# Performance work log

Hardware: AMD Instinct MI355X
Metric: run time of the kernel (lower is better)

The kernel has to match this reference:

```python
import jax, jax.numpy as jnp
import numpy as np
from jax import lax

EMBED_DIM = 512
HIDDEN_DIM = 256
OUT_DIM = HIDDEN_DIM // 2
BATCH = 32
SEQ = 4096
THRESHOLD = 1.0
DECAY = 0.95
REFRACTORY = 2.0


def setup_inputs() -> dict:
    key = jax.random.key(0)
    k1, k2, k3 = jax.random.split(key, 3)
    x = jax.random.normal(k1, (BATCH, SEQ, EMBED_DIM), dtype=jnp.float32)
    input_weights = jax.random.normal(k2, (EMBED_DIM, HIDDEN_DIM), dtype=jnp.float32) * 0.1
    hidden_weights = jax.random.normal(k3, (HIDDEN_DIM, OUT_DIM), dtype=jnp.float32) * 0.1
    return {"x": x, "input_weights": input_weights, "hidden_weights": hidden_weights}


def reference(x, input_weights, hidden_weights):
    B, S, D = x.shape
    H = input_weights.shape[1]
    dt = x.dtype
    # batch-mean then project all timesteps at once: [S, H]
    currents = jnp.einsum('sd,dh->sh', x.mean(0), input_weights)

    def step(carry, ic):
        mem, refr = carry
        active = (refr <= 0).astype(dt)
        mem = DECAY * mem + ic * active
        spikes = (mem >= THRESHOLD).astype(dt)
        mem = mem * (1.0 - spikes)
        refr = jnp.maximum(refr - 1.0, 0.0) + spikes * REFRACTORY
        return (mem, refr), spikes

    init = (jnp.zeros((H,), dt), jnp.zeros((H,), dt))
    _, spikes = lax.scan(step, init, currents)  # spikes: [S, H]
    out = spikes @ hidden_weights               # [S, OUT]
    out_mean = out.mean(0)                      # mean over timesteps
    # original repeats the (batch-independent) output across the batch
    return jnp.broadcast_to(out_mean, (B, out_mean.shape[0]))
```

## Files before the change

kernel.cpp:

```cpp
#include <hip/hip_runtime.h>
#include <stdint.h>


#define S_LEN 4096
#define D_DIM 512
#define H_DIM 256
#define O_DIM 128
#define B_SZ  32
#define TS    8
#define CH    64
#define NCH   (S_LEN / CH)
#define ROWS  (CH / 4)

typedef const __attribute__((address_space(1))) void  glob_void;
typedef       __attribute__((address_space(3))) void  lds_void;

__global__ __launch_bounds__(256)
void fused_mean_proj(const float4* __restrict__ x4,
                     const float*  __restrict__ iw,
                     float4*       __restrict__ cur4,
                     float*        __restrict__ out) {
    __shared__ float4 xm4[TS * D_DIM / 4];
    const int t   = threadIdx.x;
    const int s0  = blockIdx.x * TS;
    const int SD4 = S_LEN * D_DIM / 4;
    const size_t base = (size_t)s0 * (D_DIM / 4);

    if (blockIdx.x == 0) {
        for (int i = t; i < B_SZ * O_DIM; i += 256) out[i] = 0.f;
    }

    float4 acc[4];
    #pragma unroll
    for (int k = 0; k < 4; ++k) acc[k] = make_float4(0.f, 0.f, 0.f, 0.f);

    for (int b = 0; b < B_SZ; b += 2) {
        const float4* p0 = x4 + (size_t)b * SD4 + base;
        const float4* p1 = p0 + SD4;
        float4 v0[4], v1[4];
        #pragma unroll
        for (int k = 0; k < 4; ++k) v0[k] = p0[t + k * 256];
        #pragma unroll
        for (int k = 0; k < 4; ++k) v1[k] = p1[t + k * 256];
        #pragma unroll
        for (int k = 0; k < 4; ++k) {
            acc[k].x += v0[k].x; acc[k].y += v0[k].y; acc[k].z += v0[k].z; acc[k].w += v0[k].w;
            acc[k].x += v1[k].x; acc[k].y += v1[k].y; acc[k].z += v1[k].z; acc[k].w += v1[k].w;
        }
    }
    const float inv = 1.0f / (float)B_SZ;
    #pragma unroll
    for (int k = 0; k < 4; ++k) {
        float4 a = acc[k];
        a.x *= inv; a.y *= inv; a.z *= inv; a.w *= inv;
        xm4[t + k * 256] = a;
    }
    __syncthreads();

    const int h = t;
    float acc2[TS];
    #pragma unroll
    for (int ss = 0; ss < TS; ++ss) acc2[ss] = 0.f;

    for (int d4 = 0; d4 < D_DIM / 4; ++d4) {
        const int d = d4 * 4;
        float w0 = iw[(d + 0) * H_DIM + h];
        float w1 = iw[(d + 1) * H_DIM + h];
        float w2 = iw[(d + 2) * H_DIM + h];
        float w3 = iw[(d + 3) * H_DIM + h];
        #pragma unroll
        for (int ss = 0; ss < TS; ++ss) {
            float4 xv = xm4[ss * (D_DIM / 4) + d4];
            acc2[ss] += xv.x * w0 + xv.y * w1 + xv.z * w2 + xv.w * w3;
        }
    }
    const int g0 = (blockIdx.x * 2) * H_DIM + h;
    cur4[g0]         = make_float4(acc2[0], acc2[1], acc2[2], acc2[3]);
    cur4[g0 + H_DIM] = make_float4(acc2[4], acc2[5], acc2[6], acc2[7]);
}

#define LIF_STEP(IC) {                          \
    float ict = sp2 ? 0.f : (IC);               \
    float tt  = fmaf(0.95f, u, ict);            \
    u   = sp1 ? 0.f : tt;                       \
    bool sp = (u >= 1.0f);                      \
    cnt += sp ? 1 : 0;                          \
    sp2 = sp1; sp1 = sp; }

__global__ __launch_bounds__(64)
void snn_scan_out(const float4* __restrict__ cur4,
                  const float*  __restrict__ hw,
                  float*        __restrict__ out) {
    __shared__ __attribute__((aligned(16))) float4 lbuf[2][ROWS * 64];
    __shared__ float cl[64];
    const int lane  = threadIdx.x;
    const int hbase = blockIdx.x * 64;

    #pragma unroll
    for (int r = 0; r < ROWS; ++r) {
        const float4* g = cur4 + (size_t)r * H_DIM + hbase + lane;
        __builtin_amdgcn_global_load_lds((glob_void*)g,
                                         (lds_void*)&lbuf[0][r * 64 + lane], 16, 0, 0);
    }

    float u = 0.f;
    int   cnt = 0;
    bool  sp1 = false, sp2 = false;

    for (int c = 0; c < NCH; ++c) {
        __syncthreads();
        if (c + 1 < NCH) {
            #pragma unroll
            for (int r = 0; r < ROWS; ++r) {
                const float4* g = cur4 + (size_t)((c + 1) * ROWS + r) * H_DIM + hbase + lane;
                __builtin_amdgcn_global_load_lds((glob_void*)g,
                                                 (lds_void*)&lbuf[(c + 1) & 1][r * 64 + lane],
                                                 16, 0, 0);
            }
        }
        const float4* lb = lbuf[c & 1];
        float4 v[ROWS];
        #pragma unroll
        for (int r = 0; r < ROWS; ++r) v[r] = lb[r * 64 + lane];
        __builtin_amdgcn_sched_barrier(0);

        #pragma unroll
        for (int r = 0; r < ROWS; ++r) {
            LIF_STEP(v[r].x); LIF_STEP(v[r].y); LIF_STEP(v[r].z); LIF_STEP(v[r].w);
        }
    }

    __syncthreads();
    cl[lane] = (float)cnt;
    __syncthreads();
    float a0 = 0.f, a1 = 0.f;
    #pragma unroll 8
    for (int k = 0; k < 64; ++k) {
        float c = cl[k];
        const float* w = hw + (size_t)(hbase + k) * O_DIM;
        a0 = fmaf(c, w[lane], a0);
        a1 = fmaf(c, w[lane + 64], a1);
    }
    a0 *= (1.0f / (float)S_LEN);
    a1 *= (1.0f / (float)S_LEN);
    for (int b = 0; b < B_SZ; ++b) {
        atomicAdd(out + b * O_DIM + lane,      a0);
        atomicAdd(out + b * O_DIM + lane + 64, a1);
    }
}

extern "C" void kernel_launch(void* const* d_in, const int* in_sizes, int n_in,
                              void* d_out, int out_size, void* d_ws, size_t ws_size,
                              hipStream_t stream) {
    const float4* x4 = (const float4*)d_in[0];
    const float*  iw = (const float*) d_in[1];
    const float*  hw = (const float*) d_in[2];
    float* out   = (float*)d_out;
    float4* cur4 = (float4*)d_ws;

    hipLaunchKernelGGL(fused_mean_proj, dim3(S_LEN / TS), dim3(256), 0, stream,
                       x4, iw, cur4, out);
    hipLaunchKernelGGL(snn_scan_out, dim3(4), dim3(64), 0, stream,
                       cur4, hw, out);
}
```

Measured before the change: 471.5 us.

## Split batch-mean from projection and triple-buffer scan chunk loads

The fused mean+projection kernel is split in two. A wide batch_mean kernel (2048 blocks, 8 loads in flight per thread) streams x and writes the [S,D] mean to workspace. A separate proj kernel then reads it from global memory. The scan kernel moves from double to triple buffering with explicit vmcnt waits, prefetching two chunks ahead and dropping the per-chunk __syncthreads. This adds an extra launch and an 8MB intermediate round trip in exchange for more memory parallelism on the dominant 256MB read and more latency hiding in the serial scan.

```diff
diff --git a/kernel.cpp b/kernel.cpp
--- a/kernel.cpp
+++ b/kernel.cpp
@@ -7,7 +7,6 @@
 #define H_DIM 256
 #define O_DIM 128
 #define B_SZ  32
-#define TS    8
 #define CH    64
 #define NCH   (S_LEN / CH)
 #define ROWS  (CH / 4)
@@ -16,62 +15,50 @@
 typedef       __attribute__((address_space(3))) void  lds_void;
 
 __global__ __launch_bounds__(256)
-void fused_mean_proj(const float4* __restrict__ x4,
-                     const float*  __restrict__ iw,
-                     float4*       __restrict__ cur4,
-                     float*        __restrict__ out) {
-    __shared__ float4 xm4[TS * D_DIM / 4];
-    const int t   = threadIdx.x;
-    const int s0  = blockIdx.x * TS;
+void batch_mean(const float4* __restrict__ x4,
+                float4*       __restrict__ xm4,
+                float*        __restrict__ out) {
+    const int i = blockIdx.x * 256 + threadIdx.x;
+    if (blockIdx.x == 0) {
+        for (int k = threadIdx.x; k < B_SZ * O_DIM; k += 256) out[k] = 0.f;
+    }
     const int SD4 = S_LEN * D_DIM / 4;
-    const size_t base = (size_t)s0 * (D_DIM / 4);
-
-    if (blockIdx.x == 0) {
-        for (int i = t; i < B_SZ * O_DIM; i += 256) out[i] = 0.f;
-    }
-
-    float4 acc[4];
-    #pragma unroll
-    for (int k = 0; k < 4; ++k) acc[k] = make_float4(0.f, 0.f, 0.f, 0.f);
-
-    for (int b = 0; b < B_SZ; b += 2) {
-        const float4* p0 = x4 + (size_t)b * SD4 + base;
-        const float4* p1 = p0 + SD4;
-        float4 v0[4], v1[4];
+    const float4* p = x4 + i;
+    float4 acc = make_float4(0.f, 0.f, 0.f, 0.f);
+    for (int b = 0; b < B_SZ; b += 8) {
+        float4 q[8];
         #pragma unroll
-        for (int k = 0; k < 4; ++k) v0[k] = p0[t + k * 256];
+        for (int j = 0; j < 8; ++j) q[j] = p[(size_t)(b + j) * SD4];
         #pragma unroll
-        for (int k = 0; k < 4; ++k) v1[k] = p1[t + k * 256];
-        #pragma unroll
-        for (int k = 0; k < 4; ++k) {
-            acc[k].x += v0[k].x; acc[k].y += v0[k].y; acc[k].z += v0[k].z; acc[k].w += v0[k].w;
-            acc[k].x += v1[k].x; acc[k].y += v1[k].y; acc[k].z += v1[k].z; acc[k].w += v1[k].w;
+        for (int j = 0; j < 8; ++j) {
+            acc.x += q[j].x; acc.y += q[j].y; acc.z += q[j].z; acc.w += q[j].w;
         }
     }
     const float inv = 1.0f / (float)B_SZ;
+    acc.x *= inv; acc.y *= inv; acc.z *= inv; acc.w *= inv;
+    xm4[i] = acc;
+}
+
+__global__ __launch_bounds__(256)
+void proj(const float* __restrict__ xmean,
+          const float* __restrict__ iw,
+          float4*      __restrict__ cur4) {
+    const int h  = threadIdx.x;
+    const int s0 = blockIdx.x * 8;
+    float acc2[8];
     #pragma unroll
-    for (int k = 0; k < 4; ++k) {
-        float4 a = acc[k];
-        a.x *= inv; a.y *= inv; a.z *= inv; a.w *= inv;
-        xm4[t + k * 256] = a;
-    }
-    __syncthreads();
+    for (int ss = 0; ss < 8; ++ss) acc2[ss] = 0.f;
 
-    const int h = t;
-    float acc2[TS];
-    #pragma unroll
-    for (int ss = 0; ss < TS; ++ss) acc2[ss] = 0.f;
-
-    for (int d4 = 0; d4 < D_DIM / 4; ++d4) {
-        const int d = d4 * 4;
+    const float* xr = xmean + (size_t)s0 * D_DIM;
+    for (int d = 0; d < D_DIM; d += 4) {
         float w0 = iw[(d + 0) * H_DIM + h];
         float w1 = iw[(d + 1) * H_DIM + h];
         float w2 = iw[(d + 2) * H_DIM + h];
         float w3 = iw[(d + 3) * H_DIM + h];
         #pragma unroll
-        for (int ss = 0; ss < TS; ++ss) {
-            float4 xv = xm4[ss * (D_DIM / 4) + d4];
-            acc2[ss] += xv.x * w0 + xv.y * w1 + xv.z * w2 + xv.w * w3;
+        for (int ss = 0; ss < 8; ++ss) {
+            const float* xp = xr + ss * D_DIM + d;
+            acc2[ss] += xp[0] * w0 + xp[1] * w1 + xp[2] * w2 + xp[3] * w3;
         }
     }
     const int g0 = (blockIdx.x * 2) * H_DIM + h;
@@ -87,38 +74,45 @@
     cnt += sp ? 1 : 0;                          \
     sp2 = sp1; sp1 = sp; }
 
+__device__ __forceinline__ void stage_chunk(const float4* __restrict__ cur4,
+                                            float4* dst, int c, int hbase, int lane) {
+    #pragma unroll
+    for (int r = 0; r < ROWS; ++r) {
+        const float4* g = cur4 + (size_t)(c * ROWS + r) * H_DIM + hbase + lane;
+        __builtin_amdgcn_global_load_lds((glob_void*)g,
+                                         (lds_void*)&dst[r * 64 + lane], 16, 0, 0);
+    }
+}
+
 __global__ __launch_bounds__(64)
 void snn_scan_out(const float4* __restrict__ cur4,
                   const float*  __restrict__ hw,
                   float*        __restrict__ out) {
-    __shared__ __attribute__((aligned(16))) float4 lbuf[2][ROWS * 64];
+    __shared__ __attribute__((aligned(16))) float4 lbuf[3][ROWS * 64];
     __shared__ float cl[64];
     const int lane  = threadIdx.x;
     const int hbase = blockIdx.x * 64;
 
-    #pragma unroll
-    for (int r = 0; r < ROWS; ++r) {
-        const float4* g = cur4 + (size_t)r * H_DIM + hbase + lane;
-        __builtin_amdgcn_global_load_lds((glob_void*)g,
-                                         (lds_void*)&lbuf[0][r * 64 + lane], 16, 0, 0);
-    }
+    stage_chunk(cur4, lbuf[0], 0, hbase, lane);
+    stage_chunk(cur4, lbuf[1], 1, hbase, lane);
 
     float u = 0.f;
     int   cnt = 0;
     bool  sp1 = false, sp2 = false;
 
     for (int c = 0; c < NCH; ++c) {
-        __syncthreads();
-        if (c + 1 < NCH) {
-            #pragma unroll
-            for (int r = 0; r < ROWS; ++r) {
-                const float4* g = cur4 + (size_t)((c + 1) * ROWS + r) * H_DIM + hbase + lane;
-                __builtin_amdgcn_global_load_lds((glob_void*)g,
-                                                 (lds_void*)&lbuf[(c + 1) & 1][r * 64 + lane],
-                                                 16, 0, 0);
-            }
+        if (c + 2 < NCH) {
+            stage_chunk(cur4, lbuf[(c + 2) % 3], c + 2, hbase, lane);
+            __builtin_amdgcn_sched_barrier(0);
+            __builtin_amdgcn_s_waitcnt(0x4F70);
+            __builtin_amdgcn_sched_barrier(0);
+        } else {
+            __builtin_amdgcn_sched_barrier(0);
+            __builtin_amdgcn_s_waitcnt(0x0F70);
+            __builtin_amdgcn_sched_barrier(0);
         }
-        const float4* lb = lbuf[c & 1];
+
+        const float4* lb = lbuf[c % 3];
         float4 v[ROWS];
         #pragma unroll
         for (int r = 0; r < ROWS; ++r) v[r] = lb[r * 64 + lane];
@@ -156,10 +150,13 @@
     const float*  iw = (const float*) d_in[1];
     const float*  hw = (const float*) d_in[2];
     float* out   = (float*)d_out;
-    float4* cur4 = (float4*)d_ws;
+    float4* cur4  = (float4*)d_ws;
+    float4* xm4   = (float4*)((char*)d_ws + (size_t)4 * 1024 * 1024);
 
-    hipLaunchKernelGGL(fused_mean_proj, dim3(S_LEN / TS), dim3(256), 0, stream,
-                       x4, iw, cur4, out);
+    hipLaunchKernelGGL(batch_mean, dim3(S_LEN * D_DIM / 4 / 256), dim3(256), 0,
+                       stream, x4, xm4, out);
+    hipLaunchKernelGGL(proj, dim3(S_LEN / 8), dim3(256), 0, stream,
+                       (const float*)xm4, iw, cur4);
     hipLaunchKernelGGL(snn_scan_out, dim3(4), dim3(64), 0, stream,
                        cur4, hw, out);
 }
```

New measurement: 504.9 us. +7.1%, slower.
